# Kernel optimization log

Measured on AMD Instinct MI355X. Metric: run time of the kernel, lower is better.

## Reference

```python
import jax, jax.numpy as jnp
import numpy as np

N, E, P = 20000, 320000, 100000
TC, HID, H, OUT, PH = 256, 64, 4, 256, 512


def gat_conv(x, src, dst, n, W, a_src, a_dst, b):
    # PyG GATConv (eval, dropout=0): per-head linear, LeakyReLU(0.2) attention,
    # scatter-softmax over incoming edges, scatter-add aggregation, concat heads + bias.
    Hh, C = a_src.shape
    h = (x @ W).reshape(n, Hh, C)
    alpha_src = (h * a_src).sum(-1)  # [N, H]
    alpha_dst = (h * a_dst).sum(-1)  # [N, H]
    e = jax.nn.leaky_relu(alpha_src[src] + alpha_dst[dst], 0.2)  # [E, H]
    emax = jax.ops.segment_max(e, dst, num_segments=n)
    emax = jnp.where(jnp.isfinite(emax), emax, 0.0)
    p = jnp.exp(e - emax[dst])
    denom = jax.ops.segment_sum(p, dst, num_segments=n)
    alpha = p / jnp.maximum(denom[dst], 1e-16)  # [E, H]
    out = jax.ops.segment_sum(h[src] * alpha[:, :, None], dst, num_segments=n)  # [N, H, C]
    return out.reshape(n, Hh * C) + b


def setup_inputs() -> dict:
    key = jax.random.key(0)
    ks = jax.random.split(key, 24)
    s = 0.05
    inp = {
        "x": jax.random.normal(ks[0], (N, TC), jnp.float32),
        "edge_index": jax.random.randint(ks[1], (2, E), 0, N, jnp.int64),
        "u_nodes": jax.random.randint(ks[2], (P,), 0, N, jnp.int64),
        "v_nodes": jax.random.randint(ks[3], (P,), 0, N, jnp.int64),
        # GATConv 1: in=TC, out=HID per head, heads=H, concat
        "W1": jax.random.normal(ks[4], (TC, H * HID), jnp.float32) * s,
        "a1s": jax.random.normal(ks[5], (H, HID), jnp.float32) * s,
        "a1d": jax.random.normal(ks[6], (H, HID), jnp.float32) * s,
        "b1": jax.random.normal(ks[7], (H * HID,), jnp.float32) * s,
        # GATConv 2: in=H*HID, out=OUT, heads=1
        "W2": jax.random.normal(ks[8], (H * HID, OUT), jnp.float32) * s,
        "a2s": jax.random.normal(ks[9], (1, OUT), jnp.float32) * s,
        "a2d": jax.random.normal(ks[10], (1, OUT), jnp.float32) * s,
        "b2": jax.random.normal(ks[11], (OUT,), jnp.float32) * s,
        # gate MLP: (TC+OUT) -> (TC+OUT)//2 -> 1, Sigmoid
        "gw1": jax.random.normal(ks[12], (TC + OUT, (TC + OUT) // 2), jnp.float32) * s,
        "gb1": jax.random.normal(ks[13], ((TC + OUT) // 2,), jnp.float32) * s,
        "gw2": jax.random.normal(ks[14], ((TC + OUT) // 2, 1), jnp.float32) * s,
        "gb2": jax.random.normal(ks[15], (1,), jnp.float32) * s,
        # predictor: 2*OUT -> PH -> 1 (dropout is identity in eval)
        "pw1": jax.random.normal(ks[16], (2 * OUT, PH), jnp.float32) * s,
        "pb1": jax.random.normal(ks[17], (PH,), jnp.float32) * s,
        "pw2": jax.random.normal(ks[18], (PH, 1), jnp.float32) * s,
        "pb2": jax.random.normal(ks[19], (1,), jnp.float32) * s,
    }
    return inp


def reference(x, edge_index, u_nodes, v_nodes, W1, a1s, a1d, b1, W2, a2s, a2d, b2,
              gw1, gb1, gw2, gb2, pw1, pb1, pw2, pb2):
    n = x.shape[0]
    loops = jnp.arange(n, dtype=edge_index.dtype)
    src = jnp.concatenate([edge_index[0], loops])  # PyG GATConv adds self-loops
    dst = jnp.concatenate([edge_index[1], loops])
    h = jax.nn.elu(gat_conv(x, src, dst, n, W1, a1s, a1d, b1))
    h_graph = gat_conv(h, src, dst, n, W2, a2s, a2d, b2)
    gate_in = jnp.concatenate([x, h_graph], axis=-1)
    g = jax.nn.sigmoid(jax.nn.relu(gate_in @ gw1 + gb1) @ gw2 + gb2)  # [N,1]
    h_final = (1.0 - g) * x + g * h_graph
    pair = jnp.concatenate([h_final[u_nodes], h_final[v_nodes]], axis=-1)  # [P, 2*OUT]
    out = jax.nn.relu(pair @ pw1 + pb1) @ pw2 + pb2
    return out.squeeze(-1)
```

## Files before the change

kernel.cpp:

```cpp
#include <hip/hip_runtime.h>
#include <math.h>

#define N_NODES 20000
#define N_EDGES 320000
#define EPRIME  (N_EDGES + N_NODES)
#define NP      100000

typedef __bf16 bf16x8 __attribute__((ext_vector_type(8)));
typedef float  f32x4  __attribute__((ext_vector_type(4)));

__device__ __forceinline__ float b2f(unsigned short u) {
    union { float f; unsigned int v; } x; x.v = ((unsigned int)u) << 16; return x.f;
}
__device__ __forceinline__ unsigned short f2b(float f) {
    union { float f; unsigned int v; } x; x.f = f;
    unsigned int r = (x.v + 0x7fffu + ((x.v >> 16) & 1u)) >> 16;
    return (unsigned short)r;
}
__device__ __forceinline__ float lrelu02(float v) { return v > 0.0f ? v : 0.2f * v; }

__device__ __forceinline__ void gload16(const void* g, void* l) {
    __builtin_amdgcn_global_load_lds(
        (const __attribute__((address_space(1))) void*)g,
        (__attribute__((address_space(3))) void*)l, 16, 0, 0);
}

template<int BM, int ASRC, int EPI>
__global__ __launch_bounds__(256) void mgemm_k(
    const unsigned short* __restrict__ A0, const unsigned short* __restrict__ A1,
    const unsigned short* __restrict__ BT,
    const float* __restrict__ bias, const float* __restrict__ w2,
    unsigned short* __restrict__ Cb, float* __restrict__ outp,
    float* __restrict__ outp2,
    int M, int K, int Nn)
{
    constexpr int NJA   = BM / 64;
    constexpr int MF    = BM / 32;
    constexpr int WROWS = BM / 2;
    static_assert(NJA == 1, "counted vmcnt assumes 3 loads/stage (BM=64)");

    __shared__ unsigned short As[3][BM * 32];
    __shared__ unsigned short Bs[3][4096];

    const int tid = threadIdx.x;
    const int wave = tid >> 6, lane = tid & 63;
    const int row0 = blockIdx.x * BM, col0 = blockIdx.y * 128;
    const int ksub = (((lane & 3) ^ ((lane >> 3) & 3)) * 8);

    const unsigned short* aL;
    const unsigned short* aH;
    const unsigned short* bP[2];
    {
        const int r = wave * 16 + (lane >> 2);
        int ar = row0 + r; if (ar > M - 1) ar = M - 1;
        if (ASRC == 0) { aL = A0 + (long)ar * K;  aH = aL; }
        else           { aL = A0 + (long)ar * 256; aH = A1 + (long)ar * 256; }
    }
    #pragma unroll
    for (int j = 0; j < 2; ++j) {
        const int r = j * 64 + wave * 16 + (lane >> 2);
        bP[j] = BT + (long)(col0 + r) * K;
    }

    const int wm = wave >> 1, wn = wave & 1;
    const int lrow = lane & 15;
    const int lks = ((((lane >> 4) ^ ((lane >> 1) & 3)) & 3) * 8);

    f32x4 acc[MF][4] = {};

    const int nT = K >> 5;

    auto stage = [&](int bi, int t) {
        const int k0 = t << 5;
        const unsigned short* ga;
        if (ASRC == 0) ga = aL + k0 + ksub;
        else ga = (k0 < 256) ? (aL + k0 + ksub) : (aH + (k0 - 256) + ksub);
        gload16(ga, &As[bi][(wave * 64 + lane) * 8]);
        #pragma unroll
        for (int j = 0; j < 2; ++j)
            gload16(bP[j] + k0 + ksub, &Bs[bi][(j * 256 + wave * 64 + lane) * 8]);
    };

    stage(0, 0);
    stage(1, 1);
    for (int t = 0; t < nT; ++t) {
        if (t >= nT - 1) { asm volatile("s_waitcnt vmcnt(0)" ::: "memory"); }
        else             { asm volatile("s_waitcnt vmcnt(3)" ::: "memory"); }
        __builtin_amdgcn_sched_barrier(0);
        __builtin_amdgcn_s_barrier();
        __builtin_amdgcn_sched_barrier(0);
        if (t + 2 < nT) stage((t + 2) % 3, t + 2);
        const int buf = t % 3;
        bf16x8 a[MF], b[4];
        #pragma unroll
        for (int i = 0; i < MF; ++i)
            a[i] = *(const bf16x8*)&As[buf][(wm * WROWS + i * 16 + lrow) * 32 + lks];
        #pragma unroll
        for (int j = 0; j < 4; ++j)
            b[j] = *(const bf16x8*)&Bs[buf][(wn * 64 + j * 16 + lrow) * 32 + lks];
        asm volatile("s_waitcnt lgkmcnt(0)" ::: "memory");
        __builtin_amdgcn_sched_barrier(0);
        #pragma unroll
        for (int i = 0; i < MF; ++i)
            #pragma unroll
            for (int j = 0; j < 4; ++j)
                acc[i][j] = __builtin_amdgcn_mfma_f32_16x16x32_bf16(a[i], b[j], acc[i][j], 0, 0, 0);
    }

    if constexpr (EPI == 0 || EPI == 1 || EPI == 4 || EPI == 5) {
        #pragma unroll
        for (int i = 0; i < MF; ++i) {
            #pragma unroll
            for (int p = 0; p < 4; ++p) {
                const int row = row0 + wm * WROWS + i * 16 + (lane >> 4) * 4 + p;
                if (row < M) {
                    #pragma unroll
                    for (int j = 0; j < 4; ++j) {
                        const int col = col0 + wn * 64 + j * 16 + (lane & 15);
                        float v = acc[i][j][p];
                        if (EPI == 1) { v += bias[col]; v = v > 0.f ? v : 0.f; }
                        Cb[(long)row * Nn + col] = f2b(v);
                    }
                }
            }
        }
    }
    if constexpr (EPI == 4 || EPI == 5) {
        #pragma unroll
        for (int i = 0; i < MF; ++i) {
            #pragma unroll
            for (int p = 0; p < 4; ++p) {
                float ps = 0.f, pd = 0.f;
                #pragma unroll
                for (int j = 0; j < 4; ++j) {
                    const int col = col0 + wn * 64 + j * 16 + lrow;
                    ps = fmaf(acc[i][j][p], bias[col], ps);
                    pd = fmaf(acc[i][j][p], w2[col], pd);
                }
                #pragma unroll
                for (int off = 1; off < 16; off <<= 1) {
                    ps += __shfl_xor(ps, off);
                    pd += __shfl_xor(pd, off);
                }
                const int row = row0 + wm * WROWS + i * 16 + (lane >> 4) * 4 + p;
                if (lrow == 0 && row < M) {
                    if (EPI == 4) {
                        const int head = (col0 >> 6) + wn;
                        outp[row * 4 + head]  = ps;
                        outp2[row * 4 + head] = pd;
                    } else {
                        atomicAdd(outp + row, ps);
                        atomicAdd(outp2 + row, pd);
                    }
                }
            }
        }
    }
    if constexpr (EPI == 2) {
        float s[MF][4];
        #pragma unroll
        for (int i = 0; i < MF; ++i) {
            #pragma unroll
            for (int p = 0; p < 4; ++p) {
                float t = 0.f;
                #pragma unroll
                for (int j = 0; j < 4; ++j) {
                    const int col = col0 + wn * 64 + j * 16 + (lane & 15);
                    float v = acc[i][j][p] + bias[col];
                    v = v > 0.f ? v : 0.f;
                    t += v * w2[col];
                }
                s[i][p] = t;
            }
        }
        #pragma unroll
        for (int off = 1; off < 16; off <<= 1) {
            #pragma unroll
            for (int i = 0; i < MF; ++i)
                #pragma unroll
                for (int p = 0; p < 4; ++p)
                    s[i][p] += __shfl_xor(s[i][p], off);
        }
        if ((lane & 15) == 0) {
            #pragma unroll
            for (int i = 0; i < MF; ++i)
                #pragma unroll
                for (int p = 0; p < 4; ++p) {
                    const int row = row0 + wm * WROWS + i * 16 + (lane >> 4) * 4 + p;
                    if (row < M) atomicAdd(outp + row, s[i][p]);
                }
        }
    }
}

__global__ __launch_bounds__(512) void zgemm_k(
    const unsigned short* __restrict__ A0,
    const unsigned short* __restrict__ BT,
    const float* __restrict__ bias,
    unsigned short* __restrict__ Cb,
    int M)
{
    __shared__ unsigned short lds[36864];

    const int tid = threadIdx.x;
    const int wave = tid >> 6, lane = tid & 63;
    const int row0 = blockIdx.x * 128, col0 = blockIdx.y * 256;
    const int ksub = (((tid & 3) ^ ((tid >> 3) & 3)) * 8);

    const unsigned short* aP;
    {
        int ar = row0 + (tid >> 2); if (ar > M - 1) ar = M - 1;
        aP = A0 + (long)ar * 256;
    }
    const unsigned short* bP[2];
    #pragma unroll
    for (int j = 0; j < 2; ++j)
        bP[j] = BT + (long)(col0 + j * 128 + (tid >> 2)) * 256;

    const int wm = wave >> 2, wn = wave & 3;
    const int lrow = lane & 15, g = lane >> 4;
    const int lks = ((((lane >> 4) ^ ((lane >> 1) & 3)) & 3) * 8);

    f32x4 acc[4][4] = {};

    auto stage = [&](int bi, int t) {
        const int k0 = t << 5;
        gload16(aP + k0 + ksub, &lds[bi * 4096 + tid * 8]);
        #pragma unroll
        for (int j = 0; j < 2; ++j)
            gload16(bP[j] + k0 + ksub, &lds[12288 + bi * 8192 + (j * 512 + tid) * 8]);
    };

    stage(0, 0);
    stage(1, 1);
    #pragma unroll
    for (int t = 0; t < 8; ++t) {
        if (t >= 7) { asm volatile("s_waitcnt vmcnt(0)" ::: "memory"); }
        else        { asm volatile("s_waitcnt vmcnt(3)" ::: "memory"); }
        __builtin_amdgcn_sched_barrier(0);
        __builtin_amdgcn_s_barrier();
        __builtin_amdgcn_sched_barrier(0);
        if (t + 2 < 8) stage((t + 2) % 3, t + 2);
        const unsigned short* as_b = &lds[(t % 3) * 4096];
        const unsigned short* bs_b = &lds[12288 + (t % 3) * 8192];
        bf16x8 a[4], b[4];
        #pragma unroll
        for (int i = 0; i < 4; ++i)
            a[i] = *(const bf16x8*)&as_b[(wm * 64 + i * 16 + lrow) * 32 + lks];
        #pragma unroll
        for (int j = 0; j < 4; ++j)
            b[j] = *(const bf16x8*)&bs_b[(wn * 64 + j * 16 + lrow) * 32 + lks];
        asm volatile("s_waitcnt lgkmcnt(0)" ::: "memory");
        __builtin_amdgcn_sched_barrier(0);
        #pragma unroll
        for (int i = 0; i < 4; ++i)
            #pragma unroll
            for (int j = 0; j < 4; ++j)
                acc[i][j] = __builtin_amdgcn_mfma_f32_16x16x32_bf16(a[i], b[j], acc[i][j], 0, 0, 0);
    }
    __syncthreads();

    unsigned short* Cs = lds;
    #pragma unroll
    for (int h = 0; h < 2; ++h) {
        if (wm == h) {
            #pragma unroll
            for (int i = 0; i < 4; ++i)
                #pragma unroll
                for (int j = 0; j < 4; ++j)
                    #pragma unroll
                    for (int p = 0; p < 4; ++p) {
                        const int r = i * 16 + g * 4 + p;
                        const int c = wn * 64 + j * 16 + lrow;
                        float v = acc[i][j][p];
                        const int col = col0 + c;
                        if (col < 512) v += bias[col];
                        Cs[r * 256 + c] = f2b(v);
                    }
        }
        __syncthreads();
        #pragma unroll
        for (int q = 0; q < 4; ++q) {
            const int cq = q * 512 + tid;
            const int r = cq >> 5, ch = cq & 31;
            const int row = row0 + h * 64 + r;
            if (row < M)
                *(ulonglong2*)&Cb[(long)row * 1024 + col0 + ch * 8] =
                    *(const ulonglong2*)&Cs[r * 256 + ch * 8];
        }
        __syncthreads();
    }
}

__global__ __launch_bounds__(256) void pair_k(
    const unsigned short* __restrict__ Z, const int* __restrict__ un,
    const int* __restrict__ vn, const float* __restrict__ pw2,
    const float* __restrict__ pb2, float* __restrict__ out)
{
    const int wv = threadIdx.x >> 6, lane = threadIdx.x & 63;
    const int p = blockIdx.x * 4 + wv;
    if (p >= NP) return;
    const int u = un[p], v = vn[p];
    const int c0 = lane * 8;
    const uint4 zu = *(const uint4*)&Z[(long)u * 1024 + c0];
    const uint4 zv = *(const uint4*)&Z[(long)v * 1024 + 512 + c0];
    const float4 w2a = *(const float4*)&pw2[c0];
    const float4 w2b = *(const float4*)&pw2[c0 + 4];

    float zt[8], zb[8];
    zt[0] = b2f(zu.x & 0xffff); zt[1] = b2f(zu.x >> 16);
    zt[2] = b2f(zu.y & 0xffff); zt[3] = b2f(zu.y >> 16);
    zt[4] = b2f(zu.z & 0xffff); zt[5] = b2f(zu.z >> 16);
    zt[6] = b2f(zu.w & 0xffff); zt[7] = b2f(zu.w >> 16);
    zb[0] = b2f(zv.x & 0xffff); zb[1] = b2f(zv.x >> 16);
    zb[2] = b2f(zv.y & 0xffff); zb[3] = b2f(zv.y >> 16);
    zb[4] = b2f(zv.z & 0xffff); zb[5] = b2f(zv.z >> 16);
    zb[6] = b2f(zv.w & 0xffff); zb[7] = b2f(zv.w >> 16);

    const float ww[8] = {w2a.x, w2a.y, w2a.z, w2a.w, w2b.x, w2b.y, w2b.z, w2b.w};
    float s = 0.f;
    #pragma unroll
    for (int q = 0; q < 8; ++q) {
        float t = zt[q] + zb[q];
        t = t > 0.f ? t : 0.f;
        s = fmaf(t, ww[q], s);
    }
    #pragma unroll
    for (int off = 1; off < 64; off <<= 1) s += __shfl_xor(s, off);
    if (lane == 0) out[p] = s + pb2[0];
}

__global__ __launch_bounds__(256) void prep_k(
    const float* __restrict__ x, unsigned short* __restrict__ xb,
    const float* __restrict__ W1, unsigned short* __restrict__ W1t,
    const float* __restrict__ W2, unsigned short* __restrict__ W2t,
    const float* __restrict__ gw1, unsigned short* __restrict__ gw1t,
    const float* __restrict__ pw1, unsigned short* __restrict__ pw1t2,
    int* __restrict__ deg, float* __restrict__ gacc,
    float* __restrict__ as2v, float* __restrict__ ad2v)
{
    const int bid = blockIdx.x, tid = threadIdx.x;
    if (bid < 5000) {
        const int id = bid * 256 + tid;
        const float4 v = ((const float4*)x)[id];
        ushort4 o;
        o.x = f2b(v.x); o.y = f2b(v.y); o.z = f2b(v.z); o.w = f2b(v.w);
        ((ushort4*)xb)[id] = o;
    } else if (bid < 5256) {
        const int id = (bid - 5000) * 256 + tid;
        W1t[(id & 255) * 256 + (id >> 8)] = f2b(W1[id]);
    } else if (bid < 5512) {
        const int id = (bid - 5256) * 256 + tid;
        W2t[(id & 255) * 256 + (id >> 8)] = f2b(W2[id]);
    } else if (bid < 6024) {
        const int id = (bid - 5512) * 256 + tid;
        gw1t[(id & 255) * 512 + (id >> 8)] = f2b(gw1[id]);
    } else if (bid < 7048) {
        const int id = (bid - 6024) * 256 + tid;
        const int r = id >> 9, c = id & 511;
        const int j = (r < 256) ? c : (512 + c);
        const int k = (r < 256) ? r : (r - 256);
        pw1t2[j * 256 + k] = f2b(pw1[id]);
    } else if (bid < 7127) {
        const int i = (bid - 7048) * 256 + tid;
        if (i < N_NODES) deg[i] = 1;
    } else {
        const int i = (bid - 7127) * 256 + tid;
        if (i < 20000) gacc[i] = 0.f;
        else if (i < 40000) as2v[i - 20000] = 0.f;
        else if (i < 60000) ad2v[i - 40000] = 0.f;
    }
}

__global__ __launch_bounds__(256) void deg_count_k(const int* __restrict__ ei, int* __restrict__ deg)
{
    const int e = blockIdx.x * 256 + threadIdx.x;
    if (e < N_EDGES) atomicAdd(&deg[ei[N_EDGES + e]], 1);
}

__global__ __launch_bounds__(1024) void scan_k(const int* __restrict__ deg,
                                               int* __restrict__ indptr,
                                               int* __restrict__ pos)
{
    __shared__ int sums[1024];
    const int tid = threadIdx.x;
    const int CH = 20;
    const int start = tid * CH;
    const int end = min(start + CH, N_NODES);
    int s = 0;
    for (int i = start; i < end; ++i) s += deg[i];
    sums[tid] = s;
    __syncthreads();
    for (int off = 1; off < 1024; off <<= 1) {
        const int v = sums[tid];
        const int add = (tid >= off) ? sums[tid - off] : 0;
        __syncthreads();
        sums[tid] = v + add;
        __syncthreads();
    }
    int pre = sums[tid] - s;
    for (int i = start; i < end; ++i) {
        indptr[i] = pre;
        pos[i] = pre;
        pre += deg[i];
    }
    if (tid == 1023) indptr[N_NODES] = sums[1023];
}

__global__ __launch_bounds__(256) void fill_k(const int* __restrict__ ei,
                                              int* __restrict__ pos, int* __restrict__ csr)
{
    const int i = blockIdx.x * 256 + threadIdx.x;
    if (i < N_EDGES) {
        const int s = ei[i], d = ei[N_EDGES + i];
        const int p = atomicAdd(&pos[d], 1);
        csr[p] = s;
    } else if (i < EPRIME) {
        const int n = i - N_EDGES;
        const int p = atomicAdd(&pos[n], 1);
        csr[p] = n;
    }
}

__global__ __launch_bounds__(256) void agg1_k(
    const unsigned short* __restrict__ h1, const float* __restrict__ as1,
    const float* __restrict__ ad1, const int* __restrict__ indptr,
    const int* __restrict__ csr, const float* __restrict__ b1,
    unsigned short* __restrict__ out)
{
    __shared__ int   ssrc[4][64];
    __shared__ float sp[4][64 * 4];
    const int wv = threadIdx.x >> 6, lane = threadIdx.x & 63;
    const int n = blockIdx.x * 4 + wv;
    if (n >= N_NODES) return;

    const int beg = indptr[n], end = indptr[n + 1];
    const float4 ad = ((const float4*)ad1)[n];
    const int c0 = lane * 4;
    const int hd = lane >> 4;

    float acc[4] = {0.f, 0.f, 0.f, 0.f};
    float psum[4] = {0.f, 0.f, 0.f, 0.f};

    for (int base = beg; base < end; base += 64) {
        const int cnt = min(64, end - base);
        if (lane < cnt) {
            const int s = csr[base + lane];
            const float4 av = ((const float4*)as1)[s];
            float4 p;
            p.x = __expf(lrelu02(av.x + ad.x));
            p.y = __expf(lrelu02(av.y + ad.y));
            p.z = __expf(lrelu02(av.z + ad.z));
            p.w = __expf(lrelu02(av.w + ad.w));
            ssrc[wv][lane] = s;
            *(float4*)&sp[wv][lane * 4] = p;
            psum[0] += p.x; psum[1] += p.y; psum[2] += p.z; psum[3] += p.w;
        }
        asm volatile("s_waitcnt lgkmcnt(0)" ::: "memory");
        __builtin_amdgcn_sched_barrier(0);
        int e = 0;
        for (; e + 4 <= cnt; e += 4) {
            const int s0 = ssrc[wv][e], s1 = ssrc[wv][e + 1];
            const int s2 = ssrc[wv][e + 2], s3 = ssrc[wv][e + 3];
            const float w0 = sp[wv][(e + 0) * 4 + hd], w1 = sp[wv][(e + 1) * 4 + hd];
            const float w2v = sp[wv][(e + 2) * 4 + hd], w3 = sp[wv][(e + 3) * 4 + hd];
            const ushort4 h0 = *(const ushort4*)&h1[(long)s0 * 256 + c0];
            const ushort4 h1v = *(const ushort4*)&h1[(long)s1 * 256 + c0];
            const ushort4 h2v = *(const ushort4*)&h1[(long)s2 * 256 + c0];
            const ushort4 h3v = *(const ushort4*)&h1[(long)s3 * 256 + c0];
            acc[0] = fmaf(w0, b2f(h0.x), acc[0]);  acc[1] = fmaf(w0, b2f(h0.y), acc[1]);
            acc[2] = fmaf(w0, b2f(h0.z), acc[2]);  acc[3] = fmaf(w0, b2f(h0.w), acc[3]);
            acc[0] = fmaf(w1, b2f(h1v.x), acc[0]); acc[1] = fmaf(w1, b2f(h1v.y), acc[1]);
            acc[2] = fmaf(w1, b2f(h1v.z), acc[2]); acc[3] = fmaf(w1, b2f(h1v.w), acc[3]);
            acc[0] = fmaf(w2v, b2f(h2v.x), acc[0]); acc[1] = fmaf(w2v, b2f(h2v.y), acc[1]);
            acc[2] = fmaf(w2v, b2f(h2v.z), acc[2]); acc[3] = fmaf(w2v, b2f(h2v.w), acc[3]);
            acc[0] = fmaf(w3, b2f(h3v.x), acc[0]); acc[1] = fmaf(w3, b2f(h3v.y), acc[1]);
            acc[2] = fmaf(w3, b2f(h3v.z), acc[2]); acc[3] = fmaf(w3, b2f(h3v.w), acc[3]);
        }
        for (; e < cnt; ++e) {
            const int s = ssrc[wv][e];
            const float w = sp[wv][e * 4 + hd];
            const ushort4 hv = *(const ushort4*)&h1[(long)s * 256 + c0];
            acc[0] = fmaf(w, b2f(hv.x), acc[0]);
            acc[1] = fmaf(w, b2f(hv.y), acc[1]);
            acc[2] = fmaf(w, b2f(hv.z), acc[2]);
            acc[3] = fmaf(w, b2f(hv.w), acc[3]);
        }
        __builtin_amdgcn_sched_barrier(0);
        __builtin_amdgcn_wave_barrier();
    }

    #pragma unroll
    for (int off = 1; off < 64; off <<= 1) {
        #pragma unroll
        for (int h = 0; h < 4; ++h) psum[h] += __shfl_xor(psum[h], off);
    }
    const float invd = 1.0f / psum[hd];

    ushort4 o;
    float v;
    v = acc[0] * invd + b1[c0 + 0]; o.x = f2b(v > 0.f ? v : (__expf(v) - 1.0f));
    v = acc[1] * invd + b1[c0 + 1]; o.y = f2b(v > 0.f ? v : (__expf(v) - 1.0f));
    v = acc[2] * invd + b1[c0 + 2]; o.z = f2b(v > 0.f ? v : (__expf(v) - 1.0f));
    v = acc[3] * invd + b1[c0 + 3]; o.w = f2b(v > 0.f ? v : (__expf(v) - 1.0f));
    *(ushort4*)&out[(long)n * 256 + c0] = o;
}

__global__ __launch_bounds__(256) void agg2_k(
    const unsigned short* __restrict__ h2, const float* __restrict__ as2,
    const float* __restrict__ ad2, const int* __restrict__ indptr,
    const int* __restrict__ csr, const float* __restrict__ b2,
    unsigned short* __restrict__ outb)
{
    __shared__ int   ssrc[4][64];
    __shared__ float sp[4][64];
    const int wv = threadIdx.x >> 6, lane = threadIdx.x & 63;
    const int n = blockIdx.x * 4 + wv;
    if (n >= N_NODES) return;

    const int beg = indptr[n], end = indptr[n + 1];
    const float adv = ad2[n];
    const int c0 = lane * 4;

    float acc[4] = {0.f, 0.f, 0.f, 0.f};
    float psum = 0.f;

    for (int base = beg; base < end; base += 64) {
        const int cnt = min(64, end - base);
        if (lane < cnt) {
            const int s = csr[base + lane];
            const float p = __expf(lrelu02(as2[s] + adv));
            ssrc[wv][lane] = s;
            sp[wv][lane] = p;
            psum += p;
        }
        asm volatile("s_waitcnt lgkmcnt(0)" ::: "memory");
        __builtin_amdgcn_sched_barrier(0);
        int e = 0;
        for (; e + 4 <= cnt; e += 4) {
            const int s0 = ssrc[wv][e], s1 = ssrc[wv][e + 1];
            const int s2 = ssrc[wv][e + 2], s3 = ssrc[wv][e + 3];
            const float w0 = sp[wv][e], w1 = sp[wv][e + 1];
            const float w2v = sp[wv][e + 2], w3 = sp[wv][e + 3];
            const ushort4 h0 = *(const ushort4*)&h2[(long)s0 * 256 + c0];
            const ushort4 h1v = *(const ushort4*)&h2[(long)s1 * 256 + c0];
            const ushort4 h2u = *(const ushort4*)&h2[(long)s2 * 256 + c0];
            const ushort4 h3v = *(const ushort4*)&h2[(long)s3 * 256 + c0];
            acc[0] = fmaf(w0, b2f(h0.x), acc[0]);  acc[1] = fmaf(w0, b2f(h0.y), acc[1]);
            acc[2] = fmaf(w0, b2f(h0.z), acc[2]);  acc[3] = fmaf(w0, b2f(h0.w), acc[3]);
            acc[0] = fmaf(w1, b2f(h1v.x), acc[0]); acc[1] = fmaf(w1, b2f(h1v.y), acc[1]);
            acc[2] = fmaf(w1, b2f(h1v.z), acc[2]); acc[3] = fmaf(w1, b2f(h1v.w), acc[3]);
            acc[0] = fmaf(w2v, b2f(h2u.x), acc[0]); acc[1] = fmaf(w2v, b2f(h2u.y), acc[1]);
            acc[2] = fmaf(w2v, b2f(h2u.z), acc[2]); acc[3] = fmaf(w2v, b2f(h2u.w), acc[3]);
            acc[0] = fmaf(w3, b2f(h3v.x), acc[0]); acc[1] = fmaf(w3, b2f(h3v.y), acc[1]);
            acc[2] = fmaf(w3, b2f(h3v.z), acc[2]); acc[3] = fmaf(w3, b2f(h3v.w), acc[3]);
        }
        for (; e < cnt; ++e) {
            const int s = ssrc[wv][e];
            const float w = sp[wv][e];
            const ushort4 hv = *(const ushort4*)&h2[(long)s * 256 + c0];
            acc[0] = fmaf(w, b2f(hv.x), acc[0]);
            acc[1] = fmaf(w, b2f(hv.y), acc[1]);
            acc[2] = fmaf(w, b2f(hv.z), acc[2]);
            acc[3] = fmaf(w, b2f(hv.w), acc[3]);
        }
        __builtin_amdgcn_sched_barrier(0);
        __builtin_amdgcn_wave_barrier();
    }

    #pragma unroll
    for (int off = 1; off < 64; off <<= 1) psum += __shfl_xor(psum, off);
    const float invd = 1.0f / psum;

    ushort4 o;
    o.x = f2b(acc[0] * invd + b2[c0 + 0]);
    o.y = f2b(acc[1] * invd + b2[c0 + 1]);
    o.z = f2b(acc[2] * invd + b2[c0 + 2]);
    o.w = f2b(acc[3] * invd + b2[c0 + 3]);
    *(ushort4*)&outb[(long)n * 256 + c0] = o;
}

__global__ __launch_bounds__(256) void gatefin2_k(
    const float* __restrict__ gacc, const float* __restrict__ gb2,
    const float* __restrict__ x, const unsigned short* __restrict__ hgb,
    unsigned short* __restrict__ hfb)
{
    const int wid = threadIdx.x >> 6;
    const int lane = threadIdx.x & 63;
    const int n = blockIdx.x * 4 + wid;
    if (n >= N_NODES) return;
    const float g = 1.0f / (1.0f + __expf(-(gacc[n] + gb2[0])));
    #pragma unroll
    for (int q = 0; q < 4; ++q) {
        const int c = q * 64 + lane;
        const float xv = x[(long)n * 256 + c];
        const float hv = b2f(hgb[(long)n * 256 + c]);
        hfb[(long)n * 256 + c] = f2b((1.0f - g) * xv + g * hv);
    }
}

extern "C" void kernel_launch(void* const* d_in, const int* in_sizes, int n_in,
                              void* d_out, int out_size, void* d_ws, size_t ws_size,
                              hipStream_t stream)
{
    const float* x   = (const float*)d_in[0];
    const int*   ei  = (const int*)d_in[1];
    const int*   un  = (const int*)d_in[2];
    const int*   vn  = (const int*)d_in[3];
    const float* W1  = (const float*)d_in[4];
    const float* a1s = (const float*)d_in[5];
    const float* a1d = (const float*)d_in[6];
    const float* b1  = (const float*)d_in[7];
    const float* W2  = (const float*)d_in[8];
    const float* a2s = (const float*)d_in[9];
    const float* a2d = (const float*)d_in[10];
    const float* b2  = (const float*)d_in[11];
    const float* gw1 = (const float*)d_in[12];
    const float* gb1 = (const float*)d_in[13];
    const float* gw2 = (const float*)d_in[14];
    const float* gb2 = (const float*)d_in[15];
    const float* pw1 = (const float*)d_in[16];
    const float* pb1 = (const float*)d_in[17];
    const float* pw2 = (const float*)d_in[18];
    const float* pb2 = (const float*)d_in[19];
    float* out = (float*)d_out;

    dim3 b256(256);

    if (ws_size < 58720256u) return;

    unsigned short* Z     = (unsigned short*)d_ws;
    unsigned short* bufHb = Z;
    unsigned short* hgb   = Z + 5120000;
    unsigned short* xb    = Z + 10240000;
    unsigned short* hfb   = Z + 20480000;
    unsigned short* W1t   = hfb + 5120000;
    unsigned short* W2t   = W1t + 65536;
    unsigned short* gw1t  = W2t + 65536;
    unsigned short* pw1t2 = gw1t + 131072;
    float* as1v = (float*)(pw1t2 + 262144);
    float* ad1v = as1v + 80000;
    float* as2v = ad1v + 80000;
    float* ad2v = as2v + 20000;
    int* deg    = (int*)(ad2v + 20000);
    int* indptr = deg + 20000;
    int* pos    = indptr + 20032;
    int* csr    = pos + 20000;
    float* gacc = (float*)(csr + EPRIME);

    prep_k<<<7362, b256, 0, stream>>>(x, xb, W1, W1t, W2, W2t, gw1, gw1t,
                                      pw1, pw1t2, deg, gacc, as2v, ad2v);
    deg_count_k<<<(N_EDGES + 255) / 256, b256, 0, stream>>>(ei, deg);
    scan_k<<<1, 1024, 0, stream>>>(deg, indptr, pos);
    fill_k<<<(EPRIME + 255) / 256, b256, 0, stream>>>(ei, pos, csr);

    mgemm_k<64, 0, 4><<<dim3(313, 2), b256, 0, stream>>>(
        xb, nullptr, W1t, a1s, a1d, bufHb, as1v, ad1v, N_NODES, 256, 256);
    agg1_k<<<5000, b256, 0, stream>>>(bufHb, as1v, ad1v, indptr, csr, b1, hfb);

    mgemm_k<64, 0, 5><<<dim3(313, 2), b256, 0, stream>>>(
        hfb, nullptr, W2t, a2s, a2d, bufHb, as2v, ad2v, N_NODES, 256, 256);
    agg2_k<<<5000, b256, 0, stream>>>(bufHb, as2v, ad2v, indptr, csr, b2, hgb);

    mgemm_k<64, 1, 2><<<dim3(313, 2), b256, 0, stream>>>(
        xb, hgb, gw1t, gb1, gw2, nullptr, gacc, nullptr, N_NODES, 512, 256);
    gatefin2_k<<<5000, b256, 0, stream>>>(gacc, gb2, x, hgb, hfb);

    zgemm_k<<<dim3(157, 4), dim3(512), 0, stream>>>(hfb, pw1t2, pb1, Z, N_NODES);

    pair_k<<<25000, b256, 0, stream>>>(Z, un, vn, pw2, pb2, out);
}
```

Before: 231.0 us.

## Fuse gate blend into predictor GEMM A-operand load, drop gatefin kernel

Removes the separate gate-finalize kernel and computes the sigmoid gate and the (1-g)*x + g*h_graph blend inside the Z GEMM while staging the A tile into LDS. To allow the register round-trip, the A pipeline changes from a three-stage async global-to-LDS ring to a two-buffer register-prefetch scheme. This saves one launch and the write and re-read of the blended bf16 buffer. In exchange, each of the four column blocks re-reads fp32 x and hgb and redoes the blend, and the shallower pipeline with plain __syncthreads may expose more latency. The hgb buffer is moved in the workspace so it no longer overlaps Z, which raises the required workspace size.

New measurement: 248.0 us. +7.4%, slower.

```diff
diff --git a/kernel.cpp b/kernel.cpp
--- a/kernel.cpp
+++ b/kernel.cpp
@@ -194,55 +194,81 @@
 }
 
 __global__ __launch_bounds__(512) void zgemm_k(
-    const unsigned short* __restrict__ A0,
+    const float* __restrict__ xf,
+    const unsigned short* __restrict__ hgb,
+    const float* __restrict__ gacc, const float* __restrict__ gb2,
     const unsigned short* __restrict__ BT,
     const float* __restrict__ bias,
     unsigned short* __restrict__ Cb,
     int M)
 {
-    __shared__ unsigned short lds[36864];
+    __shared__ unsigned short lds[24576];
 
     const int tid = threadIdx.x;
     const int wave = tid >> 6, lane = tid & 63;
     const int row0 = blockIdx.x * 128, col0 = blockIdx.y * 256;
     const int ksub = (((tid & 3) ^ ((tid >> 3) & 3)) * 8);
 
-    const unsigned short* aP;
-    {
-        int ar = row0 + (tid >> 2); if (ar > M - 1) ar = M - 1;
-        aP = A0 + (long)ar * 256;
-    }
+    int ar = row0 + (tid >> 2); if (ar > M - 1) ar = M - 1;
+    const float* xP = xf + (long)ar * 256 + ksub;
+    const unsigned short* hP = hgb + (long)ar * 256 + ksub;
+    const float g = 1.0f / (1.0f + __expf(-(gacc[ar] + gb2[0])));
+
     const unsigned short* bP[2];
     #pragma unroll
     for (int j = 0; j < 2; ++j)
         bP[j] = BT + (long)(col0 + j * 128 + (tid >> 2)) * 256;
 
     const int wm = wave >> 2, wn = wave & 3;
-    const int lrow = lane & 15, g = lane >> 4;
+    const int lrow = lane & 15, gg = lane >> 4;
     const int lks = ((((lane >> 4) ^ ((lane >> 1) & 3)) & 3) * 8);
 
     f32x4 acc[4][4] = {};
 
-    auto stage = [&](int bi, int t) {
+    auto loadA = [&](int t, float4& x0, float4& x1, ushort4& h0, ushort4& h1v) {
         const int k0 = t << 5;
-        gload16(aP + k0 + ksub, &lds[bi * 4096 + tid * 8]);
+        x0  = *(const float4*)(xP + k0);
+        x1  = *(const float4*)(xP + k0 + 4);
+        h0  = *(const ushort4*)(hP + k0);
+        h1v = *(const ushort4*)(hP + k0 + 4);
+    };
+    auto writeA = [&](int bi, const float4& x0, const float4& x1,
+                      const ushort4& h0, const ushort4& h1v) {
+        uint4 o;
+        float a0, a1;
+        a0 = fmaf(g, b2f(h0.x) - x0.x, x0.x);
+        a1 = fmaf(g, b2f(h0.y) - x0.y, x0.y);
+        o.x = (unsigned)f2b(a0) | ((unsigned)f2b(a1) << 16);
+        a0 = fmaf(g, b2f(h0.z) - x0.z, x0.z);
+        a1 = fmaf(g, b2f(h0.w) - x0.w, x0.w);
+        o.y = (unsigned)f2b(a0) | ((unsigned)f2b(a1) << 16);
+        a0 = fmaf(g, b2f(h1v.x) - x1.x, x1.x);
+        a1 = fmaf(g, b2f(h1v.y) - x1.y, x1.y);
+        o.z = (unsigned)f2b(a0) | ((unsigned)f2b(a1) << 16);
+        a0 = fmaf(g, b2f(h1v.z) - x1.z, x1.z);
+        a1 = fmaf(g, b2f(h1v.w) - x1.w, x1.w);
+        o.w = (unsigned)f2b(a0) | ((unsigned)f2b(a1) << 16);
+        *(uint4*)&lds[bi * 4096 + tid * 8] = o;
+    };
+    auto stageB = [&](int bi, int t) {
+        const int k0 = t << 5;
         #pragma unroll
         for (int j = 0; j < 2; ++j)
-            gload16(bP[j] + k0 + ksub, &lds[12288 + bi * 8192 + (j * 512 + tid) * 8]);
+            gload16(bP[j] + k0 + ksub, &lds[8192 + bi * 8192 + (j * 512 + tid) * 8]);
     };
 
-    stage(0, 0);
-    stage(1, 1);
+    float4 x0, x1; ushort4 h0, h1v;
+    loadA(0, x0, x1, h0, h1v);
+    stageB(0, 0);
+    writeA(0, x0, x1, h0, h1v);
+    __syncthreads();
+
+    int buf = 0;
     #pragma unroll
     for (int t = 0; t < 8; ++t) {
-        if (t >= 7) { asm volatile("s_waitcnt vmcnt(0)" ::: "memory"); }
-        else        { asm volatile("s_waitcnt vmcnt(3)" ::: "memory"); }
-        __builtin_amdgcn_sched_barrier(0);
-        __builtin_amdgcn_s_barrier();
-        __builtin_amdgcn_sched_barrier(0);
-        if (t + 2 < 8) stage((t + 2) % 3, t + 2);
-        const unsigned short* as_b = &lds[(t % 3) * 4096];
-        const unsigned short* bs_b = &lds[12288 + (t % 3) * 8192];
+        if (t + 1 < 8) { loadA(t + 1, x0, x1, h0, h1v); stageB(buf ^ 1, t + 1); }
+        const unsigned short* as_b = &lds[buf * 4096];
+        const unsigned short* bs_b = &lds[8192 + buf * 8192];
         bf16x8 a[4], b[4];
         #pragma unroll
         for (int i = 0; i < 4; ++i)
@@ -250,15 +276,15 @@
         #pragma unroll
         for (int j = 0; j < 4; ++j)
             b[j] = *(const bf16x8*)&bs_b[(wn * 64 + j * 16 + lrow) * 32 + lks];
-        asm volatile("s_waitcnt lgkmcnt(0)" ::: "memory");
-        __builtin_amdgcn_sched_barrier(0);
         #pragma unroll
         for (int i = 0; i < 4; ++i)
             #pragma unroll
             for (int j = 0; j < 4; ++j)
                 acc[i][j] = __builtin_amdgcn_mfma_f32_16x16x32_bf16(a[i], b[j], acc[i][j], 0, 0, 0);
-    }
-    __syncthreads();
+        if (t + 1 < 8) writeA(buf ^ 1, x0, x1, h0, h1v);
+        __syncthreads();
+        buf ^= 1;
+    }
 
     unsigned short* Cs = lds;
     #pragma unroll
@@ -270,7 +296,7 @@
                 for (int j = 0; j < 4; ++j)
                     #pragma unroll
                     for (int p = 0; p < 4; ++p) {
-                        const int r = i * 16 + g * 4 + p;
+                        const int r = i * 16 + gg * 4 + p;
                         const int c = wn * 64 + j * 16 + lrow;
                         float v = acc[i][j][p];
                         const int col = col0 + c;
@@ -580,25 +606,6 @@
     *(ushort4*)&outb[(long)n * 256 + c0] = o;
 }
 
-__global__ __launch_bounds__(256) void gatefin2_k(
-    const float* __restrict__ gacc, const float* __restrict__ gb2,
-    const float* __restrict__ x, const unsigned short* __restrict__ hgb,
-    unsigned short* __restrict__ hfb)
-{
-    const int wid = threadIdx.x >> 6;
-    const int lane = threadIdx.x & 63;
-    const int n = blockIdx.x * 4 + wid;
-    if (n >= N_NODES) return;
-    const float g = 1.0f / (1.0f + __expf(-(gacc[n] + gb2[0])));
-    #pragma unroll
-    for (int q = 0; q < 4; ++q) {
-        const int c = q * 64 + lane;
-        const float xv = x[(long)n * 256 + c];
-        const float hv = b2f(hgb[(long)n * 256 + c]);
-        hfb[(long)n * 256 + c] = f2b((1.0f - g) * xv + g * hv);
-    }
-}
-
 extern "C" void kernel_launch(void* const* d_in, const int* in_sizes, int n_in,
                               void* d_out, int out_size, void* d_ws, size_t ws_size,
                               hipStream_t stream)
@@ -627,14 +634,14 @@
 
     dim3 b256(256);
 
-    if (ws_size < 58720256u) return;
+    if (ws_size < 73400320u) return;
 
     unsigned short* Z     = (unsigned short*)d_ws;
     unsigned short* bufHb = Z;
-    unsigned short* hgb   = Z + 5120000;
     unsigned short* xb    = Z + 10240000;
     unsigned short* hfb   = Z + 20480000;
-    unsigned short* W1t   = hfb + 5120000;
+    unsigned short* hgb   = hfb + 5120000;
+    unsigned short* W1t   = hgb + 5120000;
     unsigned short* W2t   = W1t + 65536;
     unsigned short* gw1t  = W2t + 65536;
     unsigned short* pw1t2 = gw1t + 131072;
@@ -664,9 +671,9 @@
 
     mgemm_k<64, 1, 2><<<dim3(313, 2), b256, 0, stream>>>(
         xb, hgb, gw1t, gb1, gw2, nullptr, gacc, nullptr, N_NODES, 512, 256);
-    gatefin2_k<<<5000, b256, 0, stream>>>(gacc, gb2, x, hgb, hfb);
-
-    zgemm_k<<<dim3(157, 4), dim3(512), 0, stream>>>(hfb, pw1t2, pb1, Z, N_NODES);
+
+    zgemm_k<<<dim3(157, 4), dim3(512), 0, stream>>>(
+        x, hgb, gacc, gb2, pw1t2, pb1, Z, N_NODES);
 
     pair_k<<<25000, b256, 0, stream>>>(Z, un, vn, pw2, pb2, out);
 }
```
